# Kernel tuning notes

Hardware: AMD Instinct MI355X
Metric: run time of the kernel (lower is better)

## Reference

```python
import jax, jax.numpy as jnp
import numpy as np

E, R, D, H = 8, 16, 2048, 8192
B, S = 2, 2048
SCALING = 2.0  # lora_alpha / r = 32 / 16


def gelu_new(x):
    # HF ACT2FN['gelu_new'] (tanh approximation), matches Phi config
    c = np.sqrt(2.0 / np.pi).astype(np.float32)
    return 0.5 * x * (1.0 + jnp.tanh(c * (x + 0.044715 * x * x * x)))


def _moe_lora(x, onehot, A, Bm):
    # x: [T,Din], A: [E,R,Din], Bm: [E,Dout,R], onehot: [T,E]
    # per-token low-rank projection for every expert (R is tiny), mask to the
    # assigned expert, then contract (e,r) jointly -> single [T,E*R]@[E*R,Dout] GEMM
    z = jnp.einsum('td,erd->ter', x, A) * onehot[:, :, None]  # [T,E,R]
    return jnp.einsum('ter,ehr->th', z, Bm)                   # [T,Dout]


def setup_inputs() -> dict:
    key = jax.random.key(0)
    ks = jax.random.split(key, 10)
    inv = lambda n: np.float32(1.0 / np.sqrt(n))
    return {
        'hidden_states': jax.random.normal(ks[0], (B, S, D), jnp.float32),
        'expert_idx': jax.random.randint(ks[1], (B, S), 0, E),
        'W1': jax.random.normal(ks[2], (H, D), jnp.float32) * inv(D),
        'b1': jax.random.normal(ks[3], (H,), jnp.float32) * 0.02,
        'A1': jax.random.normal(ks[4], (E, R, D), jnp.float32) * inv(D),
        'B1': jax.random.normal(ks[5], (E, H, R), jnp.float32) * 0.02,
        'W2': jax.random.normal(ks[6], (D, H), jnp.float32) * inv(H),
        'b2': jax.random.normal(ks[7], (D,), jnp.float32) * 0.02,
        'A2': jax.random.normal(ks[8], (E, R, H), jnp.float32) * inv(H),
        'B2': jax.random.normal(ks[9], (E, D, R), jnp.float32) * 0.02,
    }


def reference(hidden_states, expert_idx, W1, b1, A1, B1, W2, b2, A2, B2):
    b, s, d = hidden_states.shape
    x = hidden_states.reshape(b * s, d)                       # [T,D]
    onehot = jax.nn.one_hot(expert_idx.reshape(-1), A1.shape[0], dtype=x.dtype)
    # expert fc1: shared base layer + per-expert LoRA + shared bias
    h1 = x @ W1.T + b1 + SCALING * _moe_lora(x, onehot, A1, B1)
    y = gelu_new(h1)                                          # [T,H]
    # expert fc2
    out = y @ W2.T + b2 + SCALING * _moe_lora(y, onehot, A2, B2)
    return out.reshape(b, s, d)
```

## Files before the change

### kernel.cpp

```cpp
#include <hip/hip_runtime.h>
#include <hip/hip_bf16.h>
#include <math.h>

typedef __bf16 bf16_t;
typedef __bf16 bf16x4_t __attribute__((ext_vector_type(4)));
typedef __bf16 bf16x8_t __attribute__((ext_vector_type(8)));
typedef float  f32x4    __attribute__((ext_vector_type(4)));

#define NE  8
#define NR  16
#define ND  2048
#define NH  8192
#define NT  4096
#define NER 128
#define NK1 (ND + NER)
#define NK2 (NH + NER)

static __device__ __forceinline__ float gelu_fast(float x) {
    const float c2 = 1.5957691216057308f;
    float u2 = c2 * (x + 0.044715f * x * x * x);
    return x / (1.0f + __expf(-u2));
}

static __device__ __forceinline__ void load16_to_lds(const bf16_t* g, bf16_t* l) {
    __builtin_amdgcn_global_load_lds(
        (__attribute__((address_space(1))) void*)(g),
        (__attribute__((address_space(3))) void*)(l),
        16, 0, 0);
}

__global__ __launch_bounds__(256) void conv_x(
    const float* __restrict__ x, bf16_t* __restrict__ Xa1)
{
    const int i  = blockIdx.x * 256 + threadIdx.x;
    const int row = i >> 8;
    const int c8  = i & 255;
    f32x4 v0 = *(const f32x4*)(x + (long)i * 8);
    f32x4 v1 = *(const f32x4*)(x + (long)i * 8 + 4);
    bf16x8_t o = {(bf16_t)v0[0], (bf16_t)v0[1], (bf16_t)v0[2], (bf16_t)v0[3],
                  (bf16_t)v1[0], (bf16_t)v1[1], (bf16_t)v1[2], (bf16_t)v1[3]};
    *(bf16x8_t*)(Xa1 + (long)row * NK1 + (c8 << 3)) = o;
}

__global__ __launch_bounds__(256) void prep_main(
    const float* __restrict__ W, bf16_t* __restrict__ Waug,
    int ld, int shift8, int total8)
{
    const int i = blockIdx.x * 256 + threadIdx.x;
    if (i >= total8) return;
    const int row = i >> shift8;
    const int c8  = i & ((1 << shift8) - 1);
    f32x4 v0 = *(const f32x4*)(W + (long)i * 8);
    f32x4 v1 = *(const f32x4*)(W + (long)i * 8 + 4);
    bf16x8_t o = {(bf16_t)v0[0], (bf16_t)v0[1], (bf16_t)v0[2], (bf16_t)v0[3],
                  (bf16_t)v1[0], (bf16_t)v1[1], (bf16_t)v1[2], (bf16_t)v1[3]};
    *(bf16x8_t*)(Waug + (long)row * ld + (c8 << 3)) = o;
}

__global__ __launch_bounds__(256) void prep_lora(
    const float* __restrict__ Bl, bf16_t* __restrict__ Waug,
    int nrows, int K0, int ld, int total)
{
    const int i = blockIdx.x * 256 + threadIdx.x;
    if (i >= total) return;
    const int row = i >> 7;
    const int c   = i & 127;
    const int e   = c >> 4;
    const int r   = c & 15;
    float v = Bl[((long)e * nrows + row) * NR + r];
    Waug[(long)row * ld + K0 + c] = (bf16_t)v;
}

template <int SPLITS, int LD>
__global__ __launch_bounds__(256) void zred(
    const float* __restrict__ zp, const int* __restrict__ eidx,
    bf16_t* __restrict__ dst)
{
    const int i = blockIdx.x * 256 + threadIdx.x;
    const int t = i >> 7;
    const int c = i & 127;
    float s = 0.f;
#pragma unroll
    for (int j = 0; j < SPLITS; ++j) s += zp[(long)j * NT * 128 + i];
    const int e = eidx[t];
    float v = ((c >> 4) == e) ? 2.0f * s : 0.f;
    dst[(long)t * LD + c] = (bf16_t)v;
}

template <int BM, int BN, int W, int WM, int WN,
          int K, int LDA, int LDB, int LDC, int MODE>
__global__ __launch_bounds__(W * 64) void gemm_bt(
    const bf16_t* __restrict__ A,  const bf16_t* __restrict__ Bt,
    const float* __restrict__ bias, void* __restrict__ Cout)
{
    constexpr int RW  = BM / WM;
    constexpr int CW  = BN / WN;
    constexpr int MT  = RW / 16;
    constexpr int NTn = CW / 16;
    constexpr int AI  = BM / 16 / W;
    constexpr int BI  = BN / 16 / W;

    __shared__ union {
        struct { bf16_t As[2 * BM * 32]; bf16_t Bs[2 * BN * 32]; } s;
        bf16_t Cs[64 * 264];
    } u;

    const int tid   = threadIdx.x;
    const int wave  = tid >> 6;
    const int lane  = tid & 63;
    const int col16 = lane & 15;
    const int q     = lane >> 4;
    const int wm    = wave % WM;
    const int wn    = wave / WM;

    const int  rowA0 = blockIdx.y * BM;
    const int  colB0 = (MODE == 3) ? 0 : blockIdx.x * BN;
    const long koff  = (MODE == 3) ? (long)blockIdx.x * K : 0;

    const int srow  = lane >> 2;
    const int skoff = (lane & 3) * 8;

    const bf16_t* Agp[AI][2];
    const bf16_t* Bgp[BI][2];
    bf16_t*       AsD[AI][2];
    bf16_t*       BsD[BI][2];
#pragma unroll
    for (int jj = 0; jj < AI; ++jj) {
        const int j = (wave + jj * W) * 16;
#pragma unroll
        for (int h = 0; h < 2; ++h) {
            Agp[jj][h] = A + (long)(rowA0 + j + srow) * LDA + koff + h * 32 + skoff;
            AsD[jj][h] = &u.s.As[(h * BM + j) * 32];
        }
    }
#pragma unroll
    for (int jj = 0; jj < BI; ++jj) {
        const int j = (wave + jj * W) * 16;
#pragma unroll
        for (int h = 0; h < 2; ++h) {
            Bgp[jj][h] = Bt + (long)(colB0 + j + srow) * LDB + koff + h * 32 + skoff;
            BsD[jj][h] = &u.s.Bs[(h * BN + j) * 32];
        }
    }

    const bf16_t* Ard = &u.s.As[(wm * RW + col16) * 32 + q * 8];
    const bf16_t* Brd = &u.s.Bs[(wn * CW + col16) * 32 + q * 8];

    f32x4 acc[MT][NTn];
#pragma unroll
    for (int i = 0; i < MT; ++i)
#pragma unroll
        for (int j = 0; j < NTn; ++j)
            acc[i][j] = (f32x4){0.f, 0.f, 0.f, 0.f};

    for (int it = 0; it < K / 64; ++it) {
#pragma unroll
        for (int jj = 0; jj < AI; ++jj)
#pragma unroll
            for (int h = 0; h < 2; ++h) {
                load16_to_lds(Agp[jj][h], AsD[jj][h]);
                Agp[jj][h] += 64;
            }
#pragma unroll
        for (int jj = 0; jj < BI; ++jj)
#pragma unroll
            for (int h = 0; h < 2; ++h) {
                load16_to_lds(Bgp[jj][h], BsD[jj][h]);
                Bgp[jj][h] += 64;
            }
        __syncthreads();

#pragma unroll
        for (int h = 0; h < 2; ++h) {
            bf16x8_t af[MT], bfr[NTn];
#pragma unroll
            for (int mt = 0; mt < MT; ++mt)
                af[mt] = *(const bf16x8_t*)(Ard + (h * BM + mt * 16) * 32);
#pragma unroll
            for (int nt = 0; nt < NTn; ++nt)
                bfr[nt] = *(const bf16x8_t*)(Brd + (h * BN + nt * 16) * 32);
#pragma unroll
            for (int mt = 0; mt < MT; ++mt)
#pragma unroll
                for (int nt = 0; nt < NTn; ++nt)
                    acc[mt][nt] = __builtin_amdgcn_mfma_f32_16x16x32_bf16(
                        af[mt], bfr[nt], acc[mt][nt], 0, 0, 0);
        }
        __syncthreads();
    }

    if (MODE == 1) {
        float* Cf = (float*)Cout;
#pragma unroll
        for (int nt = 0; nt < NTn; ++nt) {
            const int col = colB0 + wn * CW + nt * 16 + col16;
            const float bv = bias[col];
#pragma unroll
            for (int mt = 0; mt < MT; ++mt) {
                const int row0 = rowA0 + wm * RW + mt * 16 + q * 4;
#pragma unroll
                for (int i = 0; i < 4; ++i)
                    Cf[(long)(row0 + i) * LDC + col] = acc[mt][nt][i] + bv;
            }
        }
    } else if (MODE == 3) {
        float* Cf = (float*)Cout + (long)blockIdx.x * NT * LDC;
#pragma unroll
        for (int nt = 0; nt < NTn; ++nt) {
            const int col = wn * CW + nt * 16 + col16;
#pragma unroll
            for (int mt = 0; mt < MT; ++mt) {
                const int row0 = rowA0 + wm * RW + mt * 16 + q * 4;
#pragma unroll
                for (int i = 0; i < 4; ++i)
                    Cf[(long)(row0 + i) * LDC + col] = acc[mt][nt][i];
            }
        }
    } else {
        bf16_t* Cb = (bf16_t*)Cout;
#pragma unroll
        for (int ph = 0; ph < BM / 64; ++ph) {
            const int phwm = (ph * 64) / RW;
            const int mtb  = ((ph * 64) % RW) / 16;
            if (wm == phwm) {
#pragma unroll
                for (int nt = 0; nt < NTn; ++nt) {
                    const int c = wn * CW + nt * 16 + col16;
                    const float bv = bias[colB0 + c];
#pragma unroll
                    for (int mt = 0; mt < 4; ++mt) {
                        const int rl = mt * 16 + q * 4;
#pragma unroll
                        for (int i = 0; i < 4; ++i)
                            u.Cs[(rl + i) * 264 + c] =
                                (bf16_t)gelu_fast(acc[mtb + mt][nt][i] + bv);
                    }
                }
            }
            __syncthreads();
            {
                constexpr int CPR = BN / 32;
                const int r  = tid / CPR;
                const int c0 = (tid % CPR) * 32;
                const long gbase =
                    (long)(rowA0 + ph * 64 + r) * LDC + colB0 + c0;
#pragma unroll
                for (int ch = 0; ch < 4; ++ch) {
                    bf16x8_t v = *(const bf16x8_t*)&u.Cs[r * 264 + c0 + ch * 8];
                    *(bf16x8_t*)&Cb[gbase + ch * 8] = v;
                }
            }
            __syncthreads();
        }
    }
}

extern "C" void kernel_launch(void* const* d_in, const int* in_sizes, int n_in,
                              void* d_out, int out_size, void* d_ws, size_t ws_size,
                              hipStream_t stream)
{
    const float* x    = (const float*)d_in[0];
    const int*   eidx = (const int*)  d_in[1];
    const float* W1   = (const float*)d_in[2];
    const float* b1   = (const float*)d_in[3];
    const float* A1   = (const float*)d_in[4];
    const float* B1   = (const float*)d_in[5];
    const float* W2   = (const float*)d_in[6];
    const float* b2   = (const float*)d_in[7];
    const float* A2   = (const float*)d_in[8];
    const float* B2   = (const float*)d_in[9];
    float* out = (float*)d_out;

    char* ws = (char*)d_ws;
    bf16_t* Xaug2 = (bf16_t*)(ws);
    bf16_t* Xaug1 = (bf16_t*)(ws + 68157440L);
    bf16_t* W1aug = (bf16_t*)(ws + 85983232L);
    bf16_t* W2aug = (bf16_t*)(ws + 68157440L);
    bf16_t* A1b   = (bf16_t*)(ws + 104000000L);
    bf16_t* A2b   = (bf16_t*)(ws + 104857600L);
    float*  zp1   = (float*) (ws + 106954752L);
    float*  zp2   = (float*) (ws + 85983232L);

    conv_x<<<NT * ND / 8 / 256, 256, 0, stream>>>(x, Xaug1);
    prep_main<<<(NER * ND / 8) / 256, 256, 0, stream>>>(A1, A1b, ND, 8, NER * ND / 8);
    {
        dim3 g(4, NT / 128);
        gemm_bt<128, 128, 4, 2, 2, 512, NK1, ND, 128, 3><<<g, 256, 0, stream>>>(
            Xaug1, A1b, nullptr, (void*)zp1);
    }
    zred<4, NK1><<<NT * 128 / 256, 256, 0, stream>>>(zp1, eidx, Xaug1 + ND);
    prep_main<<<(NH * ND / 8) / 256, 256, 0, stream>>>(W1, W1aug, NK1, 8, NH * ND / 8);
    prep_lora<<<(NH * NER) / 256, 256, 0, stream>>>(B1, W1aug, NH, ND, NK1, NH * NER);
    {
        dim3 g(NH / 256, NT / 256);
        gemm_bt<256, 256, 8, 2, 4, NK1, NK1, NK1, NK2, 0><<<g, 512, 0, stream>>>(
            Xaug1, W1aug, b1, (void*)Xaug2);
    }

    prep_main<<<(NER * NH / 8) / 256, 256, 0, stream>>>(A2, A2b, NH, 10, NER * NH / 8);
    {
        dim3 g(8, NT / 128);
        gemm_bt<128, 128, 4, 2, 2, 1024, NK2, NH, 128, 3><<<g, 256, 0, stream>>>(
            Xaug2, A2b, nullptr, (void*)zp2);
    }
    zred<8, NK2><<<NT * 128 / 256, 256, 0, stream>>>(zp2, eidx, Xaug2 + NH);
    prep_main<<<(ND * NH / 8) / 256, 256, 0, stream>>>(W2, W2aug, NK2, 10, ND * NH / 8);
    prep_lora<<<(ND * NER) / 256, 256, 0, stream>>>(B2, W2aug, ND, NH, NK2, ND * NER);
    {
        dim3 g(ND / 128, NT / 128);
        gemm_bt<128, 128, 4, 2, 2, NK2, NK2, NK2, ND, 1><<<g, 256, 0, stream>>>(
            Xaug2, W2aug, b2, (void*)out);
    }
}
```

Before: 604.6 us.

## Add 8-wave ping-pong pipelined GEMM kernel for both large GEMMs

Adds a new gemm8 kernel: 512 threads with a fixed 256-row block tile, a double-buffered LDS ring split into K halves, explicit vmcnt/lgkmcnt waits, barriers and setprio around MFMA phases. The goal is to overlap global-to-LDS staging with MFMA work. It replaces the fc1 GEMM and the fc2 GEMM; fc2 moves from 128x128 tiles with 256 threads to 256x128 tiles with 512 threads. The old gemm_bt is kept only for the MODE 3 z-projection. The hand-written wait counts and barriers add correctness and scheduling risk, and the larger fc2 tile halves its grid.

```diff
diff --git a/kernel.cpp b/kernel.cpp
--- a/kernel.cpp
+++ b/kernel.cpp
@@ -189,6 +189,160 @@
         __syncthreads();
     }
 
+    if (MODE == 3) {
+        float* Cf = (float*)Cout + (long)blockIdx.x * NT * LDC;
+#pragma unroll
+        for (int nt = 0; nt < NTn; ++nt) {
+            const int col = wn * CW + nt * 16 + col16;
+#pragma unroll
+            for (int mt = 0; mt < MT; ++mt) {
+                const int row0 = rowA0 + wm * RW + mt * 16 + q * 4;
+#pragma unroll
+                for (int i = 0; i < 4; ++i)
+                    Cf[(long)(row0 + i) * LDC + col] = acc[mt][nt][i];
+            }
+        }
+    }
+}
+
+
+#define BARRIER8() do { __builtin_amdgcn_sched_barrier(0); \
+    __builtin_amdgcn_s_barrier(); \
+    __builtin_amdgcn_sched_barrier(0); } while (0)
+
+#define WAITLG8() do { asm volatile("s_waitcnt lgkmcnt(0)" ::: "memory"); \
+    __builtin_amdgcn_sched_barrier(0); } while (0)
+
+template <int N>
+static __device__ __forceinline__ void wait_vm() {
+    static_assert(N == 0 || N == 3 || N == 4, "unsupported vmcnt");
+    if constexpr (N == 0) asm volatile("s_waitcnt vmcnt(0)" ::: "memory");
+    if constexpr (N == 3) asm volatile("s_waitcnt vmcnt(3)" ::: "memory");
+    if constexpr (N == 4) asm volatile("s_waitcnt vmcnt(4)" ::: "memory");
+}
+
+#define STAGE_A8(TT, KH) do { \
+    char* ld_ = smem + (((((TT) & 1) << 1) + (KH)) * ASLOT) + sdW; \
+    const bf16_t* g_ = gA + (long)(TT) * 64 + (KH) * 32; \
+    _Pragma("unroll") \
+    for (int j_ = 0; j_ < LA; ++j_) \
+        load16_to_lds(g_ + (long)j_ * 128 * LDA_, (bf16_t*)(ld_ + j_ * 8192)); \
+} while (0)
+
+#define STAGE_B8(TT, KH) do { \
+    char* ld_ = smem + BOFF0 + (((((TT) & 1) << 1) + (KH)) * BSLOT) + sdW; \
+    const bf16_t* g_ = gB + (long)(TT) * 64 + (KH) * 32; \
+    _Pragma("unroll") \
+    for (int j_ = 0; j_ < LB; ++j_) \
+        load16_to_lds(g_ + (long)j_ * 128 * LDB_, (bf16_t*)(ld_ + j_ * 8192)); \
+} while (0)
+
+#define RD_A8(RP, KH, MH) do { \
+    const char* p_ = smem + (((RP) * 2 + (KH)) * ASLOT) \
+                   + (wm * RW + (MH) * (RW / 2)) * 64 + rdoff; \
+    _Pragma("unroll") \
+    for (int mt_ = 0; mt_ < MT2; ++mt_) \
+        af[mt_] = *(const bf16x8_t*)(p_ + mt_ * 1024); \
+} while (0)
+
+#define RD_B8(RP, KH) do { \
+    const char* p_ = smem + BOFF0 + (((RP) * 2 + (KH)) * BSLOT) \
+                   + (wn * CW) * 64 + rdoff; \
+    _Pragma("unroll") \
+    for (int nt_ = 0; nt_ < NTn; ++nt_) \
+        bfr[nt_] = *(const bf16x8_t*)(p_ + nt_ * 1024); \
+} while (0)
+
+#define MFMA_PH8(MH) do { \
+    __builtin_amdgcn_s_setprio(1); \
+    _Pragma("unroll") \
+    for (int mt_ = 0; mt_ < MT2; ++mt_) \
+        _Pragma("unroll") \
+        for (int nt_ = 0; nt_ < NTn; ++nt_) \
+            acc[(MH) * MT2 + mt_][nt_] = __builtin_amdgcn_mfma_f32_16x16x32_bf16( \
+                af[mt_], bfr[nt_], acc[(MH) * MT2 + mt_][nt_], 0, 0, 0); \
+    __builtin_amdgcn_s_setprio(0); \
+} while (0)
+
+#define TILE8(T_, ST_) do { \
+    const int rp_ = (T_) & 1; \
+     \
+    RD_A8(rp_, 0, 0); RD_B8(rp_, 0); \
+    if (ST_) STAGE_A8((T_) + 1, 0); \
+    BARRIER8(); WAITLG8(); MFMA_PH8(0); BARRIER8(); \
+     \
+    RD_A8(rp_, 0, 1); \
+    if (ST_) { STAGE_B8((T_) + 1, 0); wait_vm<LA + LB>(); } \
+    else     { wait_vm<0>(); } \
+    BARRIER8(); WAITLG8(); MFMA_PH8(1); BARRIER8(); \
+     \
+    RD_A8(rp_, 1, 0); RD_B8(rp_, 1); \
+    if (ST_) STAGE_A8((T_) + 1, 1); \
+    BARRIER8(); WAITLG8(); MFMA_PH8(0); BARRIER8(); \
+     \
+    RD_A8(rp_, 1, 1); \
+    if (ST_) { STAGE_B8((T_) + 1, 1); wait_vm<LA + LB>(); } \
+    BARRIER8(); WAITLG8(); MFMA_PH8(1); BARRIER8(); \
+} while (0)
+
+template <int BN, int WM, int WN, int KT, int LDA_, int LDB_, int LDC_, int MODE>
+__global__ __launch_bounds__(512, 2) void gemm8(
+    const bf16_t* __restrict__ A, const bf16_t* __restrict__ Bt,
+    const float* __restrict__ bias, void* __restrict__ Cout)
+{
+    constexpr int BM    = 256;
+    constexpr int RW    = BM / WM;
+    constexpr int CW    = BN / WN;
+    constexpr int MT    = RW / 16;
+    constexpr int MT2   = MT / 2;
+    constexpr int NTn   = CW / 16;
+    constexpr int LA    = 2;
+    constexpr int LB    = BN / 128;
+    constexpr int NTIL  = KT / 64;
+    constexpr int ASLOT = 16384;
+    constexpr int BSLOT = BN * 64;
+    constexpr int BOFF0 = 4 * ASLOT;
+    constexpr int RING  = BOFF0 + 4 * BSLOT;
+    constexpr int CSB   = 64 * 264 * 2;
+    constexpr int SMEM  = (MODE == 0 && CSB > RING) ? CSB : RING;
+
+    __shared__ __align__(16) char smem[SMEM];
+
+    const int tid   = threadIdx.x;
+    const int wave  = tid >> 6;
+    const int lane  = tid & 63;
+    const int col16 = lane & 15;
+    const int q     = lane >> 4;
+    const int wm    = wave % WM;
+    const int wn    = wave / WM;
+
+    const int rowA0 = blockIdx.y * BM;
+    const int colB0 = blockIdx.x * BN;
+
+    const int srow = tid >> 2;
+    const int sseg = (tid & 3) ^ ((tid >> 3) & 3);
+    const bf16_t* gA = A  + (long)(rowA0 + srow) * LDA_ + sseg * 8;
+    const bf16_t* gB = Bt + (long)(colB0 + srow) * LDB_ + sseg * 8;
+    const int sdW = wave << 10;
+
+    const int rdoff = col16 * 64 + ((q ^ ((lane >> 1) & 3)) << 4);
+
+    bf16x8_t af[MT2];
+    bf16x8_t bfr[NTn];
+    f32x4 acc[MT][NTn];
+#pragma unroll
+    for (int i = 0; i < MT; ++i)
+#pragma unroll
+        for (int j = 0; j < NTn; ++j)
+            acc[i][j] = (f32x4){0.f, 0.f, 0.f, 0.f};
+
+    STAGE_A8(0, 0); STAGE_B8(0, 0); STAGE_A8(0, 1); STAGE_B8(0, 1);
+    wait_vm<LA + LB>();
+    BARRIER8();
+
+    for (int t = 0; t < NTIL - 1; ++t) TILE8(t, 1);
+    TILE8(NTIL - 1, 0);
+
     if (MODE == 1) {
         float* Cf = (float*)Cout;
 #pragma unroll
@@ -200,24 +354,12 @@
                 const int row0 = rowA0 + wm * RW + mt * 16 + q * 4;
 #pragma unroll
                 for (int i = 0; i < 4; ++i)
-                    Cf[(long)(row0 + i) * LDC + col] = acc[mt][nt][i] + bv;
-            }
-        }
-    } else if (MODE == 3) {
-        float* Cf = (float*)Cout + (long)blockIdx.x * NT * LDC;
-#pragma unroll
-        for (int nt = 0; nt < NTn; ++nt) {
-            const int col = wn * CW + nt * 16 + col16;
-#pragma unroll
-            for (int mt = 0; mt < MT; ++mt) {
-                const int row0 = rowA0 + wm * RW + mt * 16 + q * 4;
-#pragma unroll
-                for (int i = 0; i < 4; ++i)
-                    Cf[(long)(row0 + i) * LDC + col] = acc[mt][nt][i];
+                    Cf[(long)(row0 + i) * LDC_ + col] = acc[mt][nt][i] + bv;
             }
         }
     } else {
         bf16_t* Cb = (bf16_t*)Cout;
+        bf16_t* Cs = (bf16_t*)smem;
 #pragma unroll
         for (int ph = 0; ph < BM / 64; ++ph) {
             const int phwm = (ph * 64) / RW;
@@ -232,7 +374,7 @@
                         const int rl = mt * 16 + q * 4;
 #pragma unroll
                         for (int i = 0; i < 4; ++i)
-                            u.Cs[(rl + i) * 264 + c] =
+                            Cs[(rl + i) * 264 + c] =
                                 (bf16_t)gelu_fast(acc[mtb + mt][nt][i] + bv);
                     }
                 }
@@ -243,10 +385,10 @@
                 const int r  = tid / CPR;
                 const int c0 = (tid % CPR) * 32;
                 const long gbase =
-                    (long)(rowA0 + ph * 64 + r) * LDC + colB0 + c0;
+                    (long)(rowA0 + ph * 64 + r) * LDC_ + colB0 + c0;
 #pragma unroll
                 for (int ch = 0; ch < 4; ++ch) {
-                    bf16x8_t v = *(const bf16x8_t*)&u.Cs[r * 264 + c0 + ch * 8];
+                    bf16x8_t v = *(const bf16x8_t*)&Cs[r * 264 + c0 + ch * 8];
                     *(bf16x8_t*)&Cb[gbase + ch * 8] = v;
                 }
             }
@@ -293,7 +435,7 @@
     prep_lora<<<(NH * NER) / 256, 256, 0, stream>>>(B1, W1aug, NH, ND, NK1, NH * NER);
     {
         dim3 g(NH / 256, NT / 256);
-        gemm_bt<256, 256, 8, 2, 4, NK1, NK1, NK1, NK2, 0><<<g, 512, 0, stream>>>(
+        gemm8<256, 2, 4, NK1, NK1, NK1, NK2, 0><<<g, 512, 0, stream>>>(
             Xaug1, W1aug, b1, (void*)Xaug2);
     }
 
@@ -307,8 +449,8 @@
     prep_main<<<(ND * NH / 8) / 256, 256, 0, stream>>>(W2, W2aug, NK2, 10, ND * NH / 8);
     prep_lora<<<(ND * NER) / 256, 256, 0, stream>>>(B2, W2aug, ND, NH, NK2, ND * NER);
     {
-        dim3 g(ND / 128, NT / 128);
-        gemm_bt<128, 128, 4, 2, 2, NK2, NK2, NK2, ND, 1><<<g, 256, 0, stream>>>(
+        dim3 g(ND / 128, NT / 256);
+        gemm8<128, 4, 2, NK2, NK2, NK2, ND, 1><<<g, 512, 0, stream>>>(
             Xaug2, W2aug, b2, (void*)out);
     }
 }
```

New measurement: 550.9 us. 1.1x faster.
